# Performance work log

Measured on AMD Instinct MI355X. Metric: run time of the kernel, lower is better.

The kernel has to match this reference:

```python
import jax, jax.numpy as jnp
import numpy as np

N = 100000  # nodes
E = 1600000  # edges
D_IN, D_HID, D_OUT = 128, 128, 64
NEG_SLOPE = 0.2


def gat_conv(x, src, dst, W_src, W_dst, att_src, att_dst, bias, num_nodes):
    # PyG GATConv, heads=1, add_self_loops=False.
    h_src = x @ W_src          # [N, C]
    h_dst = x @ W_dst          # [N, C]
    a_src = (h_src * att_src).sum(-1)   # [N]
    a_dst = (h_dst * att_dst).sum(-1)   # [N]
    logits = jax.nn.leaky_relu(a_src[src] + a_dst[dst], NEG_SLOPE)  # [E]
    # segment softmax over destination neighborhoods
    seg_max = jax.ops.segment_max(logits, dst, num_segments=num_nodes)  # [N]
    e = jnp.exp(logits - seg_max[dst])
    denom = jax.ops.segment_sum(e, dst, num_segments=num_nodes)         # [N]
    alpha = e / (denom[dst] + 1e-16)                                    # [E]
    out = jax.ops.segment_sum(alpha[:, None] * h_src[src], dst, num_segments=num_nodes)  # [N, C]
    return out + bias


def setup_inputs() -> dict:
    key = jax.random.key(0)
    ks = jax.random.split(key, 12)
    x = jax.random.normal(ks[0], (N, D_IN), dtype=jnp.float32)
    edge_index = jax.random.randint(ks[1], (2, E), 0, N, dtype=jnp.int64)
    s1 = 1.0 / np.sqrt(D_IN)
    s2 = 1.0 / np.sqrt(D_HID)
    return {
        "x": x,
        "edge_index": edge_index,
        "W1_src": jax.random.uniform(ks[2], (D_IN, D_HID), jnp.float32, -s1, s1),
        "W1_dst": jax.random.uniform(ks[3], (D_IN, D_HID), jnp.float32, -s1, s1),
        "att1_src": jax.random.uniform(ks[4], (D_HID,), jnp.float32, -s2, s2),
        "att1_dst": jax.random.uniform(ks[5], (D_HID,), jnp.float32, -s2, s2),
        "b1": jnp.zeros((D_HID,), jnp.float32),
        "W2_src": jax.random.uniform(ks[6], (D_HID, D_OUT), jnp.float32, -s2, s2),
        "W2_dst": jax.random.uniform(ks[7], (D_HID, D_OUT), jnp.float32, -s2, s2),
        "att2_src": jax.random.uniform(ks[8], (D_OUT,), jnp.float32, -1.0 / np.sqrt(D_OUT), 1.0 / np.sqrt(D_OUT)),
        "att2_dst": jax.random.uniform(ks[9], (D_OUT,), jnp.float32, -1.0 / np.sqrt(D_OUT), 1.0 / np.sqrt(D_OUT)),
        "b2": jnp.zeros((D_OUT,), jnp.float32),
    }


def reference(x, edge_index, W1_src, W1_dst, att1_src, att1_dst, b1,
              W2_src, W2_dst, att2_src, att2_dst, b2):
    src, dst = edge_index[0], edge_index[1]
    h = gat_conv(x, src, dst, W1_src, W1_dst, att1_src, att1_dst, b1, N)
    h = jax.nn.relu(h)
    out = gat_conv(h, src, dst, W2_src, W2_dst, att2_src, att2_dst, b2, N)
    return out
```

## Files before the change

kernel.cpp:

```cpp
#include <hip/hip_runtime.h>


typedef unsigned long long u64;
typedef float v4f __attribute__((ext_vector_type(4)));
typedef _Float16 v2h __attribute__((ext_vector_type(2)));
typedef __fp16 h8 __attribute__((ext_vector_type(8)));

#define SEL_LO 0x01000504u
#define SEL_HI 0x03020706u

__device__ __forceinline__ void ntstore4(float* p, v4f v) {
    __builtin_nontemporal_store(v, (v4f*)p);
}
__device__ __forceinline__ unsigned h2pack(float a, float b) {
    v2h h;
    h.x = (_Float16)a;
    h.y = (_Float16)b;
    return __builtin_bit_cast(unsigned, h);
}
__device__ __forceinline__ float fdot2u(unsigned u, v2h w, float acc) {
    return __builtin_amdgcn_fdot2(__builtin_bit_cast(v2h, u), w, acc, false);
}
__device__ __forceinline__ v2h pkrtz(float a, float b) {
    return __builtin_bit_cast(v2h, __builtin_amdgcn_cvt_pkrtz(a, b));
}

__device__ void matvec_body(const float* __restrict__ W, const float* __restrict__ a,
                            float* __restrict__ out, int cols, int row) {
    int lane = threadIdx.x & 63;
    float s = 0.f;
    for (int j = lane; j < cols; j += 64) s += W[row * cols + j] * a[j];
#pragma unroll
    for (int o = 32; o; o >>= 1) s += __shfl_xor(s, o, 64);
    if (lane == 0) out[row] = s;
}

template <int C>
__device__ void packw_body(const float* __restrict__ W, uint4* __restrict__ Wp) {
    constexpr int NT = C / 16;
    const int total = 4 * NT * 64;
    for (int e = threadIdx.x; e < total; e += 256) {
        int lane = e & 63;
        int ti = (e >> 6) % NT;
        int t = (e >> 6) / NT;
        int k0 = 32 * t + (lane >> 4) * 8;
        int n = ti * 16 + (lane & 15);
        unsigned u[4];
#pragma unroll
        for (int p = 0; p < 4; ++p)
            u[p] = h2pack(W[(size_t)(k0 + 2 * p) * C + n], W[(size_t)(k0 + 2 * p + 1) * C + n]);
        Wp[e] = make_uint4(u[0], u[1], u[2], u[3]);
    }
}

__global__ __launch_bounds__(256) void setup_kernel(
    const int* __restrict__ dst, int* __restrict__ gh, int E, int nbE,
    const float* __restrict__ W1s, uint4* __restrict__ wp1,
    const float* __restrict__ W2s, uint4* __restrict__ wp2,
    const float* __restrict__ W1d, const float* __restrict__ att1d, float* __restrict__ watt1,
    const float* __restrict__ W2d, const float* __restrict__ att2d, float* __restrict__ watt2) {
    int b = blockIdx.x;
    if (b < nbE) {
        __shared__ int h[256];
        h[threadIdx.x] = 0;
        __syncthreads();
        int base = b * 4096;
        int lim = min(base + 4096, E);
        for (int i = base + threadIdx.x; i < lim; i += 256)
            atomicAdd(&h[__builtin_nontemporal_load(dst + i) >> 9], 1);
        __syncthreads();
        int v = h[threadIdx.x];
        if (v) atomicAdd(&gh[threadIdx.x], v);
    } else if (b == nbE) {
        packw_body<128>(W1s, wp1);
    } else if (b == nbE + 1) {
        packw_body<64>(W2s, wp2);
    } else if (b < nbE + 34) {
        matvec_body(W1d, att1d, watt1, 128, (b - nbE - 2) * 4 + (threadIdx.x >> 6));
    } else {
        matvec_body(W2d, att2d, watt2, 64, (b - nbE - 34) * 4 + (threadIdx.x >> 6));
    }
}

__global__ __launch_bounds__(256) void bscan_kernel(const int* __restrict__ gh,
                                                    int* __restrict__ bbase,
                                                    int* __restrict__ gcur,
                                                    int* __restrict__ offs, int N, int E) {
    __shared__ int s[256];
    int t = threadIdx.x;
    int v = gh[t];
    s[t] = v;
    __syncthreads();
    for (int o = 1; o < 256; o <<= 1) {
        int u = (t >= o) ? s[t - o] : 0;
        __syncthreads();
        s[t] += u;
        __syncthreads();
    }
    int excl = s[t] - v;
    bbase[t] = excl;
    gcur[t] = excl;
    if (t == 255) { bbase[256] = E; offs[N] = E; }
}

__device__ void scatter_body(const int* __restrict__ src, const int* __restrict__ dst,
                             int* __restrict__ gcur, unsigned* __restrict__ pairs, int E,
                             int blk, char* smem) {
    int* h = (int*)smem;
    int* sbase = h + 256;
    int* rbase = h + 512;
    unsigned* buf = (unsigned*)(smem + 3072);
    unsigned char* b8 = (unsigned char*)(smem + 19456);
    const int tid = threadIdx.x;
    h[tid] = 0;
    __syncthreads();
    const int base = blk * 4096;
    const int lim = min(4096, E - base);
    unsigned pv[16];
    int rk[16];
    int bk[16];
#pragma unroll 16
    for (int k = 0; k < 16; ++k) {
        int i = base + k * 256 + tid;
        if (i < E) {
            int d = __builtin_nontemporal_load(dst + i);
            int b = d >> 9;
            bk[k] = b;
            pv[k] = ((unsigned)(d & 511) << 17) |
                    (unsigned)__builtin_nontemporal_load(src + i);
            rk[k] = atomicAdd(&h[b], 1);
        } else {
            bk[k] = -1;
        }
    }
    __syncthreads();
    const int v = h[tid];
    sbase[tid] = v;
    __syncthreads();
    for (int o = 1; o < 256; o <<= 1) {
        int uu = (tid >= o) ? sbase[tid - o] : 0;
        __syncthreads();
        sbase[tid] += uu;
        __syncthreads();
    }
    const int excl = sbase[tid] - v;
    rbase[tid] = v ? atomicAdd(&gcur[tid], v) : 0;
    __syncthreads();
    sbase[tid] = excl;
    __syncthreads();
#pragma unroll 16
    for (int k = 0; k < 16; ++k)
        if (bk[k] >= 0) {
            int pos = sbase[bk[k]] + rk[k];
            buf[pos] = pv[k];
            b8[pos] = (unsigned char)bk[k];
        }
    __syncthreads();
    for (int i = tid; i < lim; i += 256) {
        unsigned p = buf[i];
        int b = b8[i];
        __builtin_nontemporal_store(p, pairs + (size_t)rbase[b] + (i - sbase[b]));
    }
}

__global__ __launch_bounds__(512) void bsort_kernel(const unsigned* __restrict__ pairs,
                                                    const int* __restrict__ bbase,
                                                    int* __restrict__ offs,
                                                    int* __restrict__ srcs, int N) {
    __shared__ int h[512];
    __shared__ int cur[512];
    const int t = threadIdx.x;
    const int b = blockIdx.x;
    const int beg = bbase[b], end = bbase[b + 1];
    h[t] = 0;
    __syncthreads();
    for (int i = beg + t; i < end; i += 512)
        atomicAdd(&h[__builtin_nontemporal_load(pairs + i) >> 17], 1);
    __syncthreads();
    int v = h[t];
    cur[t] = v;
    __syncthreads();
    for (int o = 1; o < 512; o <<= 1) {
        int u = (t >= o) ? cur[t - o] : 0;
        __syncthreads();
        cur[t] += u;
        __syncthreads();
    }
    int pos0 = beg + cur[t] - v;
    __syncthreads();
    cur[t] = pos0;
    int g = (b << 9) + t;
    if (g < N) offs[g] = pos0;
    __syncthreads();
    for (int i = beg + t; i < end; i += 512) {
        unsigned p = __builtin_nontemporal_load(pairs + i);
        int local = (int)(p >> 17);
        int pp = atomicAdd(&cur[local], 1);
        srcs[pp] = (int)(p & 0x1FFFFu);
    }
}

template <int C, bool XF16>
__device__ void gemm_body(int blk, const void* __restrict__ Xv, const uint4* __restrict__ Wp,
                          const float* __restrict__ attS, const float* __restrict__ wda,
                          unsigned* __restrict__ H, float* __restrict__ aS,
                          float* __restrict__ aD, int M, _Float16* hsAll) {
    constexpr int NT = C / 16;
    const int tid = threadIdx.x;
    const int w = tid >> 6;
    const int lane = tid & 63;
    const int l15 = lane & 15;
    const int q = lane >> 4;
    const int mb = blk * 64 + w * 16;
    const int m = mb + l15;
    const bool mv = m < M;

    v4f acc[NT];
#pragma unroll
    for (int n = 0; n < NT; ++n) acc[n] = (v4f)(0.f);
    float pd = 0.f;
    uint4 afu[4];

    if constexpr (XF16) {
        const uint4* Xp = (const uint4*)Xv + (size_t)m * 16;
#pragma unroll
        for (int t = 0; t < 4; ++t) {
            uint4 u = make_uint4(0u, 0u, 0u, 0u);
            if (mv) u = Xp[4 * t + q];
            afu[t] = u;
            const float* wdp = wda + 32 * t + 8 * q;
            pd = fdot2u(u.x, pkrtz(wdp[0], wdp[1]), pd);
            pd = fdot2u(u.y, pkrtz(wdp[2], wdp[3]), pd);
            pd = fdot2u(u.z, pkrtz(wdp[4], wdp[5]), pd);
            pd = fdot2u(u.w, pkrtz(wdp[6], wdp[7]), pd);
        }
    } else {
        const float* Xp = (const float*)Xv + (size_t)m * 128;
#pragma unroll
        for (int t = 0; t < 4; ++t) {
            float4 x0 = make_float4(0.f, 0.f, 0.f, 0.f);
            float4 x1 = x0;
            if (mv) {
                x0 = *(const float4*)(Xp + 32 * t + 8 * q);
                x1 = *(const float4*)(Xp + 32 * t + 8 * q + 4);
            }
            const float* wdp = wda + 32 * t + 8 * q;
            pd += x0.x * wdp[0] + x0.y * wdp[1] + x0.z * wdp[2] + x0.w * wdp[3] +
                  x1.x * wdp[4] + x1.y * wdp[5] + x1.z * wdp[6] + x1.w * wdp[7];
            afu[t] = make_uint4(h2pack(x0.x, x0.y), h2pack(x0.z, x0.w),
                                h2pack(x1.x, x1.y), h2pack(x1.z, x1.w));
        }
    }

#pragma unroll
    for (int t = 0; t < 4; ++t) {
        h8 a = __builtin_bit_cast(h8, afu[t]);
        const uint4* wp = Wp + (size_t)t * NT * 64 + lane;
#pragma unroll
        for (int n = 0; n < NT; ++n) {
            h8 b = __builtin_bit_cast(h8, wp[n * 64]);
            acc[n] = __builtin_amdgcn_mfma_f32_16x16x32_f16(a, b, acc[n], 0, 0, 0);
        }
    }

    pd += __shfl_xor(pd, 16, 64);
    pd += __shfl_xor(pd, 32, 64);
    if (q == 0 && mv) aD[m] = pd;

    float as4[4] = {0.f, 0.f, 0.f, 0.f};
#pragma unroll
    for (int n = 0; n < NT; ++n) {
        float av = attS[n * 16 + l15];
#pragma unroll
        for (int r = 0; r < 4; ++r) as4[r] += acc[n][r] * av;
    }
#pragma unroll
    for (int r = 0; r < 4; ++r) {
#pragma unroll
        for (int o = 1; o < 16; o <<= 1) as4[r] += __shfl_xor(as4[r], o, 64);
    }
    if (l15 == 0) {
#pragma unroll
        for (int r = 0; r < 4; ++r) {
            int row = mb + q * 4 + r;
            if (row < M) aS[row] = as4[r];
        }
    }

    _Float16* hp = hsAll + w * (16 * 136);
#pragma unroll
    for (int n = 0; n < NT; ++n)
#pragma unroll
        for (int r = 0; r < 4; ++r)
            hp[(q * 4 + r) * 136 + n * 16 + l15] = (_Float16)acc[n][r];

    constexpr int CH = C / 32;
    if (lane < 16 * CH) {
        int row = lane / CH;
        int ch = lane % CH;
        const uint4* rp = (const uint4*)(hp + row * 136 + ch * 32);
        uint4 v0 = rp[0], v1 = rp[1], v2 = rp[2], v3 = rp[3];
        int gr = mb + row;
        if (gr < M) {
            uint4* op = (uint4*)(H + (size_t)gr * (C / 2)) + ch * 4;
            op[0] = v0; op[1] = v1; op[2] = v2; op[3] = v3;
        }
    }
}

__global__ __launch_bounds__(256) void scatter_gemm_kernel(
    const int* __restrict__ src, const int* __restrict__ dst, int* __restrict__ gcur,
    unsigned* __restrict__ pairs, int E, int nbS,
    const void* __restrict__ Xv, const uint4* __restrict__ Wp,
    const float* __restrict__ attS, const float* __restrict__ wda,
    unsigned* __restrict__ H, float* __restrict__ aS, float* __restrict__ aD, int M) {
    __shared__ __align__(16) char smem[23552];
    int b = blockIdx.x;
    if (b < nbS) scatter_body(src, dst, gcur, pairs, E, b, smem);
    else gemm_body<128, false>(b - nbS, Xv, Wp, attS, wda, H, aS, aD, M, (_Float16*)smem);
}

template <int C, bool RELU, bool F16OUT, bool NTOUT>
__global__ __launch_bounds__(256) void aggregate_kernel(
    const int* __restrict__ offs, const int* __restrict__ srcs,
    const unsigned* __restrict__ hsrc, const float* __restrict__ aS,
    const float* __restrict__ aD, const float* __restrict__ bias,
    void* __restrict__ outv, int n) {
    const int lane = threadIdx.x & 63;
    const int sl = lane & 31;
    const int hb = lane & 32;
    const int g = (lane >> 4) & 1;
    const int l = lane & 15;
    int node = (int)((blockIdx.x * blockDim.x + threadIdx.x) >> 5);
    if (node >= n) return;

    const int beg = offs[node], end = offs[node + 1];
    const int deg = end - beg;
    const float ad = aD[node];

    constexpr int LW = C / 32;
    constexpr int NA = C / 16;
    float acc[NA];
#pragma unroll
    for (int i = 0; i < NA; ++i) acc[i] = 0.f;

    int sj = 0;
    float u = 0.f;

    auto ldrow = [&](int s, unsigned* r) {
        if constexpr (C == 128) {
            uint4 v = ((const uint4*)(hsrc + ((size_t)s << 6)))[l];
            r[0] = v.x; r[1] = v.y; r[2] = v.z; r[3] = v.w;
        } else {
            uint2 v = ((const uint2*)(hsrc + ((size_t)s << 5)))[l];
            r[0] = v.x; r[1] = v.y;
        }
    };
    auto issue = [&](int j, unsigned (*buf)[LW]) {
        int e0 = hb + j * 8 + g;
        int s0 = __shfl(sj, e0, 64);
        int s1 = __shfl(sj, e0 + 2, 64);
        int s2 = __shfl(sj, e0 + 4, 64);
        int s3 = __shfl(sj, e0 + 6, 64);
        ldrow(s0, buf[0]);
        ldrow(s1, buf[1]);
        ldrow(s2, buf[2]);
        ldrow(s3, buf[3]);
    };
    auto compute = [&](int j, unsigned (*buf)[LW], float inv) {
        int e0 = hb + j * 8 + g;
        float w0 = __shfl(u, e0, 64) * inv, w1 = __shfl(u, e0 + 2, 64) * inv;
        float w2 = __shfl(u, e0 + 4, 64) * inv, w3 = __shfl(u, e0 + 6, 64) * inv;
        v2h w01 = pkrtz(w0, w1);
        v2h w23 = pkrtz(w2, w3);
#pragma unroll
        for (int ii = 0; ii < LW; ++ii) {
            acc[2 * ii] = fdot2u(__builtin_amdgcn_perm(buf[0][ii], buf[1][ii], SEL_LO), w01,
                          fdot2u(__builtin_amdgcn_perm(buf[2][ii], buf[3][ii], SEL_LO), w23, acc[2 * ii]));
            acc[2 * ii + 1] = fdot2u(__builtin_amdgcn_perm(buf[0][ii], buf[1][ii], SEL_HI), w01,
                              fdot2u(__builtin_amdgcn_perm(buf[2][ii], buf[3][ii], SEL_HI), w23, acc[2 * ii + 1]));
        }
    };

    unsigned A0[4][LW], A1[4][LW];

    if (deg <= 32) {
        int i = beg + sl;
        if (i < end) {
            sj = __builtin_nontemporal_load(srcs + i);
            float lg = aS[sj] + ad;
            lg = (lg > 0.f) ? lg : 0.2f * lg;
            u = __expf(lg);
        }
        int jm = (deg + 7) >> 3;
        if (jm > 0) issue(0, A0);
        if (jm > 1) issue(1, A1);
        float s = u;
#pragma unroll
        for (int o = 16; o; o >>= 1) s += __shfl_xor(s, o, 64);
        float inv = 1.f / (s + 1e-16f);
        if (jm > 0) { compute(0, A0, inv); if (jm > 2) issue(2, A0); }
        if (jm > 1) { compute(1, A1, inv); if (jm > 3) issue(3, A1); }
        if (jm > 2) compute(2, A0, inv);
        if (jm > 3) compute(3, A1, inv);
    } else {
        float m = -INFINITY;
        for (int i = beg + sl; i < end; i += 32) {
            float lg = aS[srcs[i]] + ad;
            lg = (lg > 0.f) ? lg : 0.2f * lg;
            m = fmaxf(m, lg);
        }
#pragma unroll
        for (int o = 16; o; o >>= 1) m = fmaxf(m, __shfl_xor(m, o, 64));
        float ssum = 0.f;
        for (int i = beg + sl; i < end; i += 32) {
            float lg = aS[srcs[i]] + ad;
            lg = (lg > 0.f) ? lg : 0.2f * lg;
            ssum += __expf(lg - m);
        }
#pragma unroll
        for (int o = 16; o; o >>= 1) ssum += __shfl_xor(ssum, o, 64);
        float inv = 1.f / (ssum + 1e-16f);
        for (int base = beg; base < end; base += 32) {
            int i = base + sl;
            sj = 0;
            u = 0.f;
            if (i < end) {
                sj = srcs[i];
                float lg = aS[sj] + ad;
                lg = (lg > 0.f) ? lg : 0.2f * lg;
                u = __expf(lg - m);
            }
            int cnt = min(32, end - base);
            int cj = (cnt + 7) >> 3;
            if (cj > 0) issue(0, A0);
            if (cj > 1) issue(1, A1);
            if (cj > 0) { compute(0, A0, inv); if (cj > 2) issue(2, A0); }
            if (cj > 1) { compute(1, A1, inv); if (cj > 3) issue(3, A1); }
            if (cj > 2) compute(2, A0, inv);
            if (cj > 3) compute(3, A1, inv);
        }
    }

#pragma unroll
    for (int i = 0; i < NA; ++i) acc[i] += __shfl_xor(acc[i], 16, 64);

    if (sl < 16) {
        float o[NA];
        const float* bp = bias + l * NA;
#pragma unroll
        for (int i = 0; i < NA; ++i) {
            o[i] = acc[i] + bp[i];
            if (RELU) o[i] = fmaxf(o[i], 0.f);
        }
        if constexpr (F16OUT) {
            unsigned uo[NA / 2];
#pragma unroll
            for (int k = 0; k < NA / 2; ++k) uo[k] = h2pack(o[2 * k], o[2 * k + 1]);
            unsigned* op = (unsigned*)outv + (size_t)node * (C / 2) + l * (NA / 2);
            if constexpr (NA == 8) *(uint4*)op = make_uint4(uo[0], uo[1], uo[2], uo[3]);
            else *(uint2*)op = make_uint2(uo[0], uo[1]);
        } else {
            float* op = (float*)outv + (size_t)node * C + l * NA;
#pragma unroll
            for (int q = 0; q < NA / 4; ++q) {
                v4f ov;
                ov.x = o[q * 4 + 0]; ov.y = o[q * 4 + 1];
                ov.z = o[q * 4 + 2]; ov.w = o[q * 4 + 3];
                if (NTOUT) ntstore4(op + q * 4, ov);
                else *(v4f*)(op + q * 4) = ov;
            }
        }
    }
}

__global__ __launch_bounds__(512) void agg_gemm_kernel(
    const int* __restrict__ offs, const int* __restrict__ srcs,
    const unsigned* __restrict__ hsrc, const float* __restrict__ aS,
    const float* __restrict__ aD, const float* __restrict__ bias,
    const uint4* __restrict__ Wp2, const float* __restrict__ attS2,
    const float* __restrict__ wda2, unsigned* __restrict__ g2h,
    float* __restrict__ aS2, float* __restrict__ aD2, int n) {
    __shared__ __align__(16) _Float16 lds[64 * 136];
    const int tid = threadIdx.x;
    const int lane = tid & 63;
    const int sl = lane & 31;
    const int hb = lane & 32;
    const int g = (lane >> 4) & 1;
    const int l = lane & 15;
    const int nodeBase = blockIdx.x * 64;

    if (nodeBase + 64 > n) {
        for (int i = tid; i < 64 * 136 / 2; i += 512) ((unsigned*)lds)[i] = 0u;
        __syncthreads();
    }

    constexpr int LW = 4;
    constexpr int NA = 8;

    for (int k = 0; k < 4; ++k) {
        const int row = k * 16 + (tid >> 5);
        const int node = nodeBase + row;
        if (node < n) {
            const int beg = offs[node], end = offs[node + 1];
            const int deg = end - beg;
            const float ad = aD[node];
            float acc[NA];
#pragma unroll
            for (int i = 0; i < NA; ++i) acc[i] = 0.f;
            int sj = 0;
            float u = 0.f;

            auto ldrow = [&](int s, unsigned* r) {
                uint4 v = ((const uint4*)(hsrc + ((size_t)s << 6)))[l];
                r[0] = v.x; r[1] = v.y; r[2] = v.z; r[3] = v.w;
            };
            auto issue = [&](int j, unsigned (*buf)[LW]) {
                int e0 = hb + j * 8 + g;
                int s0 = __shfl(sj, e0, 64);
                int s1 = __shfl(sj, e0 + 2, 64);
                int s2 = __shfl(sj, e0 + 4, 64);
                int s3 = __shfl(sj, e0 + 6, 64);
                ldrow(s0, buf[0]);
                ldrow(s1, buf[1]);
                ldrow(s2, buf[2]);
                ldrow(s3, buf[3]);
            };
            auto compute = [&](int j, unsigned (*buf)[LW], float inv) {
                int e0 = hb + j * 8 + g;
                float w0 = __shfl(u, e0, 64) * inv, w1 = __shfl(u, e0 + 2, 64) * inv;
                float w2 = __shfl(u, e0 + 4, 64) * inv, w3 = __shfl(u, e0 + 6, 64) * inv;
                v2h w01 = pkrtz(w0, w1);
                v2h w23 = pkrtz(w2, w3);
#pragma unroll
                for (int ii = 0; ii < LW; ++ii) {
                    acc[2 * ii] = fdot2u(__builtin_amdgcn_perm(buf[0][ii], buf[1][ii], SEL_LO), w01,
                                  fdot2u(__builtin_amdgcn_perm(buf[2][ii], buf[3][ii], SEL_LO), w23, acc[2 * ii]));
                    acc[2 * ii + 1] = fdot2u(__builtin_amdgcn_perm(buf[0][ii], buf[1][ii], SEL_HI), w01,
                                     fdot2u(__builtin_amdgcn_perm(buf[2][ii], buf[3][ii], SEL_HI), w23, acc[2 * ii + 1]));
                }
            };

            unsigned A0[4][LW], A1[4][LW];

            if (deg <= 32) {
                int i = beg + sl;
                if (i < end) {
                    sj = __builtin_nontemporal_load(srcs + i);
                    float lg = aS[sj] + ad;
                    lg = (lg > 0.f) ? lg : 0.2f * lg;
                    u = __expf(lg);
                }
                int jm = (deg + 7) >> 3;
                if (jm > 0) issue(0, A0);
                if (jm > 1) issue(1, A1);
                float s = u;
#pragma unroll
                for (int o = 16; o; o >>= 1) s += __shfl_xor(s, o, 64);
                float inv = 1.f / (s + 1e-16f);
                if (jm > 0) { compute(0, A0, inv); if (jm > 2) issue(2, A0); }
                if (jm > 1) { compute(1, A1, inv); if (jm > 3) issue(3, A1); }
                if (jm > 2) compute(2, A0, inv);
                if (jm > 3) compute(3, A1, inv);
            } else {
                float m = -INFINITY;
                for (int i = beg + sl; i < end; i += 32) {
                    float lg = aS[srcs[i]] + ad;
                    lg = (lg > 0.f) ? lg : 0.2f * lg;
                    m = fmaxf(m, lg);
                }
#pragma unroll
                for (int o = 16; o; o >>= 1) m = fmaxf(m, __shfl_xor(m, o, 64));
                float ssum = 0.f;
                for (int i = beg + sl; i < end; i += 32) {
                    float lg = aS[srcs[i]] + ad;
                    lg = (lg > 0.f) ? lg : 0.2f * lg;
                    ssum += __expf(lg - m);
                }
#pragma unroll
                for (int o = 16; o; o >>= 1) ssum += __shfl_xor(ssum, o, 64);
                float inv = 1.f / (ssum + 1e-16f);
                for (int base = beg; base < end; base += 32) {
                    int i = base + sl;
                    sj = 0;
                    u = 0.f;
                    if (i < end) {
                        sj = srcs[i];
                        float lg = aS[sj] + ad;
                        lg = (lg > 0.f) ? lg : 0.2f * lg;
                        u = __expf(lg - m);
                    }
                    int cnt = min(32, end - base);
                    int cj = (cnt + 7) >> 3;
                    if (cj > 0) issue(0, A0);
                    if (cj > 1) issue(1, A1);
                    if (cj > 0) { compute(0, A0, inv); if (cj > 2) issue(2, A0); }
                    if (cj > 1) { compute(1, A1, inv); if (cj > 3) issue(3, A1); }
                    if (cj > 2) compute(2, A0, inv);
                    if (cj > 3) compute(3, A1, inv);
                }
            }

#pragma unroll
            for (int i = 0; i < NA; ++i) acc[i] += __shfl_xor(acc[i], 16, 64);

            if (sl < 16) {
                float o[NA];
                const float* bp = bias + l * NA;
#pragma unroll
                for (int i = 0; i < NA; ++i) o[i] = fmaxf(acc[i] + bp[i], 0.f);
                unsigned uo[4];
#pragma unroll
                for (int kk = 0; kk < 4; ++kk) uo[kk] = h2pack(o[2 * kk], o[2 * kk + 1]);
                unsigned* op = (unsigned*)(lds + (size_t)row * 136) + l * 4;
                *(uint4*)op = make_uint4(uo[0], uo[1], uo[2], uo[3]);
            }
        }
    }
    __syncthreads();

    const int w = tid >> 6;
    if (w >= 4) return;
    const int l15 = lane & 15;
    const int q = lane >> 4;
    const int mb = nodeBase + w * 16;
    const int m = mb + l15;
    const bool mv = m < n;
    const _Float16* xrow = lds + (size_t)(w * 16 + l15) * 136;

    v4f acc2[4];
#pragma unroll
    for (int nn = 0; nn < 4; ++nn) acc2[nn] = (v4f)(0.f);
    float pd = 0.f;
    uint4 afu[4];
#pragma unroll
    for (int t = 0; t < 4; ++t) {
        uint4 u = ((const uint4*)xrow)[4 * t + q];
        afu[t] = u;
        const float* wdp = wda2 + 32 * t + 8 * q;
        pd = fdot2u(u.x, pkrtz(wdp[0], wdp[1]), pd);
        pd = fdot2u(u.y, pkrtz(wdp[2], wdp[3]), pd);
        pd = fdot2u(u.z, pkrtz(wdp[4], wdp[5]), pd);
        pd = fdot2u(u.w, pkrtz(wdp[6], wdp[7]), pd);
    }
#pragma unroll
    for (int t = 0; t < 4; ++t) {
        h8 a = __builtin_bit_cast(h8, afu[t]);
        const uint4* wp = Wp2 + (size_t)t * 4 * 64 + lane;
#pragma unroll
        for (int nn = 0; nn < 4; ++nn) {
            h8 b = __builtin_bit_cast(h8, wp[nn * 64]);
            acc2[nn] = __builtin_amdgcn_mfma_f32_16x16x32_f16(a, b, acc2[nn], 0, 0, 0);
        }
    }

    pd += __shfl_xor(pd, 16, 64);
    pd += __shfl_xor(pd, 32, 64);
    if (q == 0 && mv) aD2[m] = pd;

    float as4[4] = {0.f, 0.f, 0.f, 0.f};
#pragma unroll
    for (int nn = 0; nn < 4; ++nn) {
        float av = attS2[nn * 16 + l15];
#pragma unroll
        for (int r = 0; r < 4; ++r) as4[r] += acc2[nn][r] * av;
    }
#pragma unroll
    for (int r = 0; r < 4; ++r) {
#pragma unroll
        for (int o = 1; o < 16; o <<= 1) as4[r] += __shfl_xor(as4[r], o, 64);
    }
    if (l15 == 0) {
#pragma unroll
        for (int r = 0; r < 4; ++r) {
            int row = mb + q * 4 + r;
            if (row < n) aS2[row] = as4[r];
        }
    }

    _Float16* hp = lds + (size_t)w * (16 * 136);
#pragma unroll
    for (int nn = 0; nn < 4; ++nn)
#pragma unroll
        for (int r = 0; r < 4; ++r)
            hp[(q * 4 + r) * 136 + nn * 16 + l15] = (_Float16)acc2[nn][r];

    if (lane < 32) {
        int row = lane >> 1;
        int ch = lane & 1;
        const uint4* rp = (const uint4*)(hp + row * 136 + ch * 32);
        uint4 v0 = rp[0], v1 = rp[1], v2 = rp[2], v3 = rp[3];
        int gr = mb + row;
        if (gr < n) {
            uint4* op = (uint4*)(g2h + (size_t)gr * 32) + ch * 4;
            op[0] = v0; op[1] = v1; op[2] = v2; op[3] = v3;
        }
    }
}

extern "C" void kernel_launch(void* const* d_in, const int* in_sizes, int n_in,
                              void* d_out, int out_size, void* d_ws, size_t ws_size,
                              hipStream_t stream) {
    const float* x     = (const float*)d_in[0];
    const int*   edge  = (const int*)d_in[1];
    const float* W1s   = (const float*)d_in[2];
    const float* W1d   = (const float*)d_in[3];
    const float* att1s = (const float*)d_in[4];
    const float* att1d = (const float*)d_in[5];
    const float* b1    = (const float*)d_in[6];
    const float* W2s   = (const float*)d_in[7];
    const float* W2d   = (const float*)d_in[8];
    const float* att2s = (const float*)d_in[9];
    const float* att2d = (const float*)d_in[10];
    const float* b2    = (const float*)d_in[11];

    const int N = in_sizes[0] / 128;
    const int E = in_sizes[1] / 2;
    const int* srcI = edge;
    const int* dstI = edge + E;

    const int nbE = (E + 4095) / 4096;
    const int nbuckets = (N + 511) >> 9;
    const int gblk = (N + 63) / 64;

    size_t off = 0;
    auto alloc = [&](size_t bytes) {
        void* p = (char*)d_ws + off;
        off += (bytes + 255) & ~(size_t)255;
        return p;
    };
    int*      offs  = (int*)alloc((size_t)(N + 1) * 4);
    int*      srcs  = (int*)alloc((size_t)E * 4);
    int*      gh    = (int*)alloc(256 * 4);
    int*      bbase = (int*)alloc(257 * 4);
    int*      gcur  = (int*)alloc(256 * 4);
    float*    watt1 = (float*)alloc(128 * 4);
    float*    watt2 = (float*)alloc(128 * 4);
    uint4*    wp1   = (uint4*)alloc(4 * 8 * 64 * 16);
    uint4*    wp2   = (uint4*)alloc(4 * 4 * 64 * 16);
    float*    a_s   = (float*)alloc((size_t)N * 4);
    float*    a_d   = (float*)alloc((size_t)N * 4);
    float*    a_s2  = (float*)alloc((size_t)N * 4);
    float*    a_d2  = (float*)alloc((size_t)N * 4);
    unsigned* g1h   = (unsigned*)alloc((size_t)N * 128 * 2);
    unsigned* g2h   = (unsigned*)alloc((size_t)N * 64 * 2);
    unsigned* pairs = (unsigned*)g2h;

    hipMemsetAsync(gh, 0, 256 * 4, stream);
    setup_kernel<<<nbE + 66, 256, 0, stream>>>(dstI, gh, E, nbE, W1s, wp1, W2s, wp2,
                                               W1d, att1d, watt1, W2d, att2d, watt2);
    bscan_kernel<<<1, 256, 0, stream>>>(gh, bbase, gcur, offs, N, E);
    scatter_gemm_kernel<<<nbE + gblk, 256, 0, stream>>>(srcI, dstI, gcur, pairs, E, nbE,
                                                        x, wp1, att1s, watt1, g1h, a_s, a_d, N);
    bsort_kernel<<<nbuckets, 512, 0, stream>>>(pairs, bbase, offs, srcs, N);
    agg_gemm_kernel<<<gblk, 512, 0, stream>>>(offs, srcs, g1h, a_s, a_d, b1,
                                              wp2, att2s, watt2, g2h, a_s2, a_d2, N);
    aggregate_kernel<64, false, false, true><<<(N + 7) / 8, 256, 0, stream>>>(
        offs, srcs, g2h, a_s2, a_d2, b2, d_out, N);
}
```

Before: 285.8 us.

## Replace global histogram atomics with per-block histograms and balance agg rows dynamically

The setup kernel now writes each block's 256-bucket histogram to its own slot, and the scan kernel sums those slots. This removes the memset launch and the global atomics. In agg_gemm_kernel, each half-wave now takes node rows from a shared LDS counter instead of a fixed 4-row assignment, so high-degree nodes no longer leave other half-waves idle. The cost is a longer serial reduction loop in the single-block scan (about 391 blocks) and one LDS atomic plus shuffle per row.

```diff
diff --git a/kernel.cpp b/kernel.cpp
--- a/kernel.cpp
+++ b/kernel.cpp
@@ -54,7 +54,7 @@
 }
 
 __global__ __launch_bounds__(256) void setup_kernel(
-    const int* __restrict__ dst, int* __restrict__ gh, int E, int nbE,
+    const int* __restrict__ dst, int* __restrict__ hist, int E, int nbE,
     const float* __restrict__ W1s, uint4* __restrict__ wp1,
     const float* __restrict__ W2s, uint4* __restrict__ wp2,
     const float* __restrict__ W1d, const float* __restrict__ att1d, float* __restrict__ watt1,
@@ -69,8 +69,7 @@
         for (int i = base + threadIdx.x; i < lim; i += 256)
             atomicAdd(&h[__builtin_nontemporal_load(dst + i) >> 9], 1);
         __syncthreads();
-        int v = h[threadIdx.x];
-        if (v) atomicAdd(&gh[threadIdx.x], v);
+        __builtin_nontemporal_store(h[threadIdx.x], hist + b * 256 + threadIdx.x);
     } else if (b == nbE) {
         packw_body<128>(W1s, wp1);
     } else if (b == nbE + 1) {
@@ -82,13 +81,15 @@
     }
 }
 
-__global__ __launch_bounds__(256) void bscan_kernel(const int* __restrict__ gh,
+__global__ __launch_bounds__(256) void bscan_kernel(const int* __restrict__ hist, int nbE,
                                                     int* __restrict__ bbase,
                                                     int* __restrict__ gcur,
                                                     int* __restrict__ offs, int N, int E) {
     __shared__ int s[256];
     int t = threadIdx.x;
-    int v = gh[t];
+    int v = 0;
+#pragma unroll 4
+    for (int b = 0; b < nbE; ++b) v += hist[b * 256 + t];
     s[t] = v;
     __syncthreads();
     for (int o = 1; o < 256; o <<= 1) {
@@ -482,6 +483,7 @@
     const float* __restrict__ wda2, unsigned* __restrict__ g2h,
     float* __restrict__ aS2, float* __restrict__ aD2, int n) {
     __shared__ __align__(16) _Float16 lds[64 * 136];
+    __shared__ int ctr;
     const int tid = threadIdx.x;
     const int lane = tid & 63;
     const int sl = lane & 31;
@@ -490,17 +492,21 @@
     const int l = lane & 15;
     const int nodeBase = blockIdx.x * 64;
 
+    if (tid == 0) ctr = 0;
     if (nodeBase + 64 > n) {
         for (int i = tid; i < 64 * 136 / 2; i += 512) ((unsigned*)lds)[i] = 0u;
-        __syncthreads();
-    }
+    }
+    __syncthreads();
 
     constexpr int LW = 4;
     constexpr int NA = 8;
 
-    for (int k = 0; k < 4; ++k) {
-        const int row = k * 16 + (tid >> 5);
-        const int node = nodeBase + row;
+    for (;;) {
+        int idx = 0;
+        if (sl == 0) idx = atomicAdd(&ctr, 1);
+        idx = __shfl(idx, hb, 64);
+        if (idx >= 64) break;
+        const int node = nodeBase + idx;
         if (node < n) {
             const int beg = offs[node], end = offs[node + 1];
             const int deg = end - beg;
@@ -612,7 +618,7 @@
                 unsigned uo[4];
 #pragma unroll
                 for (int kk = 0; kk < 4; ++kk) uo[kk] = h2pack(o[2 * kk], o[2 * kk + 1]);
-                unsigned* op = (unsigned*)(lds + (size_t)row * 136) + l * 4;
+                unsigned* op = (unsigned*)(lds + (size_t)idx * 136) + l * 4;
                 *(uint4*)op = make_uint4(uo[0], uo[1], uo[2], uo[3]);
             }
         }
@@ -731,7 +737,7 @@
     };
     int*      offs  = (int*)alloc((size_t)(N + 1) * 4);
     int*      srcs  = (int*)alloc((size_t)E * 4);
-    int*      gh    = (int*)alloc(256 * 4);
+    int*      hist  = (int*)alloc((size_t)nbE * 256 * 4);
     int*      bbase = (int*)alloc(257 * 4);
     int*      gcur  = (int*)alloc(256 * 4);
     float*    watt1 = (float*)alloc(128 * 4);
@@ -746,10 +752,9 @@
     unsigned* g2h   = (unsigned*)alloc((size_t)N * 64 * 2);
     unsigned* pairs = (unsigned*)g2h;
 
-    hipMemsetAsync(gh, 0, 256 * 4, stream);
-    setup_kernel<<<nbE + 66, 256, 0, stream>>>(dstI, gh, E, nbE, W1s, wp1, W2s, wp2,
+    setup_kernel<<<nbE + 66, 256, 0, stream>>>(dstI, hist, E, nbE, W1s, wp1, W2s, wp2,
                                                W1d, att1d, watt1, W2d, att2d, watt2);
-    bscan_kernel<<<1, 256, 0, stream>>>(gh, bbase, gcur, offs, N, E);
+    bscan_kernel<<<1, 256, 0, stream>>>(hist, nbE, bbase, gcur, offs, N, E);
     scatter_gemm_kernel<<<nbE + gblk, 256, 0, stream>>>(srcI, dstI, gcur, pairs, E, nbE,
                                                         x, wp1, att1s, watt1, g1h, a_s, a_d, N);
     bsort_kernel<<<nbuckets, 512, 0, stream>>>(pairs, bbase, offs, srcs, N);
```

After: 325.5 us. +13.9%, slower.
